# Optimization experiments

Measured on AMD Instinct MI355X. Metric: run time of the kernel, lower is better.

The kernel has to match this reference:

```python
import jax, jax.numpy as jnp
import numpy as np
from jax import lax

D_MODEL = 1024
D_STATE = 128
HEADDIM = 64
EXPAND = 2
NGROUPS = 1
CHUNK = 256
D_INNER = EXPAND * D_MODEL          # 2048
D_SSM = D_INNER                      # d_ssm defaults to d_inner
NHEADS = D_SSM // HEADDIM            # 32
CONV_DIM = D_SSM + 2 * NGROUPS * D_STATE   # 2304
D_IN_PROJ = 2 * D_INNER + 2 * NGROUPS * D_STATE + NHEADS  # 4384 -> d_mlp = 0
BATCH = 2
SEQLEN = 2048
EPS = 1e-5


def setup_inputs() -> dict:
    key = jax.random.key(0)
    ks = jax.random.split(key, 9)
    u = jax.random.normal(ks[0], (BATCH, SEQLEN, D_MODEL), jnp.float32)
    # indices into left-padded (len = SEQLEN+1) sequence; 0 selects the zero pad
    conv_indices = jax.random.randint(ks[1], (BATCH, 4 * SEQLEN), 0, SEQLEN + 1)
    W_in = jax.random.normal(ks[2], (D_IN_PROJ, D_MODEL), jnp.float32) / np.sqrt(D_MODEL).astype(np.float32)
    conv_w = jax.random.normal(ks[3], (CONV_DIM, 4), jnp.float32) * 0.2
    conv_b = jax.random.normal(ks[4], (CONV_DIM,), jnp.float32) * 0.02
    # dt_bias init exactly as the module: inverse-softplus of dt in [dt_min, dt_max]
    dt = jnp.exp(jax.random.uniform(ks[5], (NHEADS,), jnp.float32) * (np.log(0.1) - np.log(0.001)) + np.log(0.001))
    dt = jnp.clip(dt, 1e-4)
    dt_bias = dt + jnp.log(-jnp.expm1(-dt))
    A_log = jnp.log(jax.random.uniform(ks[6], (NHEADS,), jnp.float32, minval=1.0, maxval=16.0))
    D = jnp.ones((NHEADS,), jnp.float32)
    norm_w = jnp.ones((D_SSM,), jnp.float32)
    W_out = jax.random.normal(ks[7], (D_MODEL, D_INNER), jnp.float32) / np.sqrt(D_INNER).astype(np.float32)
    return dict(u=u, conv_indices=conv_indices, W_in=W_in, conv_w=conv_w, conv_b=conv_b,
                dt_bias=dt_bias, A_log=A_log, D=D, norm_w=norm_w, W_out=W_out)


def _segsum(x):
    # x: (b, c, h, cs) -> (b, c, h, cs, cs); out[..., t, s] = sum_{k=s+1..t} x[..., k]
    cs = x.shape[-1]
    cx = jnp.cumsum(x, axis=-1)
    diff = cx[..., :, None] - cx[..., None, :]
    mask = jnp.tril(jnp.ones((cs, cs), dtype=bool))
    return jnp.where(mask, diff, -jnp.inf)


def _ssd(x, dt, A, Bh, Ch, D):
    # Mamba2 SSD chunked scan. x:(b,l,h,p), dt:(b,l,h), A:(h,), Bh/Ch:(b,l,h,n), D:(h,)
    b, l, h, p = x.shape
    n = Bh.shape[-1]
    c = l // CHUNK
    xr = x.reshape(b, c, CHUNK, h, p)
    dtr = dt.reshape(b, c, CHUNK, h)
    Br = Bh.reshape(b, c, CHUNK, h, n)
    Cr = Ch.reshape(b, c, CHUNK, h, n)
    dA = dtr * A                                 # (b,c,cs,h)
    Acum = jnp.cumsum(dA, axis=2)                # (b,c,cs,h)
    Lm = jnp.exp(_segsum(jnp.transpose(dA, (0, 1, 3, 2))))  # (b,c,h,cs,cs)
    dtx = xr * dtr[..., None]                    # dt-weighted inputs
    # intra-chunk (diagonal blocks)
    Yd = jnp.einsum('bcthn,bcshn,bchts,bcshp->bcthp', Cr, Br, Lm, dtx)
    # per-chunk final states
    decay_states = jnp.exp(Acum[:, :, -1:, :] - Acum)        # (b,c,cs,h)
    states = jnp.einsum('bcshn,bcsh,bcshp->bchpn', Br, decay_states, dtx)
    chunk_decay = jnp.exp(Acum[:, :, -1, :])     # (b,c,h)
    def step(h_prev, inp):
        dec, st = inp
        return h_prev * dec[..., None, None] + st, h_prev
    init = jnp.zeros((b, h, p, n), x.dtype)
    _, prev = lax.scan(step, init, (jnp.moveaxis(chunk_decay, 1, 0), jnp.moveaxis(states, 1, 0)))
    prev = jnp.moveaxis(prev, 0, 1)              # (b,c,h,p,n): state entering each chunk
    # inter-chunk (off-diagonal) contribution
    Yoff = jnp.einsum('bcthn,bchpn,bcth->bcthp', Cr, prev, jnp.exp(Acum))
    Y = Yd + Yoff + D[None, None, None, :, None] * xr
    return Y.reshape(b, l, h, p)


def reference(u, conv_indices, W_in, conv_w, conv_b, dt_bias, A_log, D, norm_w, W_out):
    b, l, _ = u.shape
    zxbcdt = u @ W_in.T                          # (b,l,4384); d_mlp == 0
    z, xBC, dt_raw = jnp.split(zxbcdt, [D_SSM, D_SSM + CONV_DIM], axis=-1)
    # tree conv: left-pad seq by 1, gather 4 tree positions per output step, depthwise conv k=4 stride=4
    xc = jnp.transpose(xBC, (0, 2, 1))           # (b, conv_dim, l)
    xp = jnp.pad(xc, ((0, 0), (0, 0), (1, 0)))
    idx = jnp.broadcast_to(conv_indices[:, None, :], (b, CONV_DIM, 4 * l))
    g = jnp.take_along_axis(xp, idx, axis=2).reshape(b, CONV_DIM, l, 4)
    conv = jnp.einsum('bclk,ck->bcl', g, conv_w) + conv_b[None, :, None]
    xBC = jax.nn.silu(jnp.transpose(conv, (0, 2, 1)))  # (b,l,conv_dim)
    x, Bm, Cm = jnp.split(xBC, [D_SSM, D_SSM + NGROUPS * D_STATE], axis=-1)
    x = x.reshape(b, l, NHEADS, HEADDIM)
    hpg = NHEADS // NGROUPS
    Bh = jnp.repeat(Bm.reshape(b, l, NGROUPS, D_STATE), hpg, axis=2)
    Ch = jnp.repeat(Cm.reshape(b, l, NGROUPS, D_STATE), hpg, axis=2)
    dt = jax.nn.softplus(dt_raw + dt_bias)       # dt_softplus=True, default dt_limit
    A = -jnp.exp(A_log.astype(jnp.float32))
    y = _ssd(x, dt, A, Bh, Ch, D).reshape(b, l, D_SSM)
    # RMSNormGated, norm_before_gate=False, group_size = d_ssm (ngroups=1)
    yz = y * jax.nn.silu(z)
    var = jnp.mean(jnp.square(yz), axis=-1, keepdims=True)
    y = yz * lax.rsqrt(var + EPS) * norm_w
    return y @ W_out.T
```

## Files before the change

kernel.cpp:

```cpp
#include <hip/hip_runtime.h>

#define BB 2
#define LL 2048
#define DMODEL 1024
#define DSSM 2048
#define NH 32
#define HD 64
#define DST 128
#define CONVD 2304
#define DPROJ 4384
#define CS 64
#define NC 32
#define BLTOT (BB*LL)

typedef short v8s __attribute__((ext_vector_type(8)));
typedef float v4f __attribute__((ext_vector_type(4)));

__device__ __forceinline__ float b2f(unsigned short h) {
  union { unsigned int u; float f; } v; v.u = ((unsigned int)h) << 16; return v.f;
}
__device__ __forceinline__ unsigned short f2b(float f) {
  union { float f; unsigned int u; } v; v.f = f;
  unsigned int u = v.u;
  return (unsigned short)((u + 0x7fffu + ((u >> 16) & 1u)) >> 16);
}
__device__ __forceinline__ v4f mfma16(v8s a, v8s b, v4f c) {
  return __builtin_amdgcn_mfma_f32_16x16x32_bf16(a, b, c, 0, 0, 0);
}
__device__ __forceinline__ void gl_lds16(const unsigned short* g, unsigned short* l) {
  __builtin_amdgcn_global_load_lds(
      (const __attribute__((address_space(1))) void*)(g),
      (__attribute__((address_space(3))) void*)(l), 16, 0, 0);
}

__global__ __launch_bounds__(256) void cvt3_kernel(
    const float* __restrict__ a, unsigned short* __restrict__ oa, int na4,
    const float* __restrict__ b, unsigned short* __restrict__ ob, int nb4,
    const float* __restrict__ c, unsigned short* __restrict__ oc, int nc4)
{
  int i = blockIdx.x * 256 + threadIdx.x;
  const float* src; unsigned short* dst; int j;
  if (i < na4) { src = a; dst = oa; j = i; }
  else if (i < na4 + nb4) { src = b; dst = ob; j = i - na4; }
  else if (i < na4 + nb4 + nc4) { src = c; dst = oc; j = i - na4 - nb4; }
  else return;
  float4 v = ((const float4*)src)[j];
  ushort4 o;
  o.x = f2b(v.x); o.y = f2b(v.y); o.z = f2b(v.z); o.w = f2b(v.w);
  ((ushort4*)dst)[j] = o;
}

template<int TN, int OUT_BF16, int DBUF>
__global__ __launch_bounds__(256) void gemm_bt(
    const unsigned short* __restrict__ A, const unsigned short* __restrict__ Bt,
    void* __restrict__ Cout, int M, int N, int K, int ldc)
{
  constexpr int NT = TN / 32;
  constexpr int NB = DBUF ? 2 : 1;
  const int bm = blockIdx.x, bn = blockIdx.y;
  const int tid = threadIdx.x;
  const int wave = tid >> 6, lane = tid & 63;
  const int wm = wave & 1, wn = wave >> 1;
  const int q = lane >> 4, lr = lane & 15;

  __shared__ __align__(16) unsigned short As[NB][128 * 64];
  __shared__ __align__(16) unsigned short Bs[NB][TN * 64];

  v4f acc[4][NT];
#pragma unroll
  for (int i = 0; i < 4; i++)
#pragma unroll
    for (int j = 0; j < NT; j++) acc[i][j] = v4f{0.f, 0.f, 0.f, 0.f};

  const int lrow = lane >> 3;
  const int gchunk = (lane & 7) ^ lrow;

#define STAGE_TILE(bufi, k0) do {                                              \
    _Pragma("unroll")                                                          \
    for (int it = 0; it < 4; ++it) {                                           \
      int r = wave * 32 + it * 8 + lrow;                                       \
      gl_lds16(A + (size_t)(bm * 128 + r) * K + (k0) + gchunk * 8,             \
               &As[bufi][(wave * 32 + it * 8) * 64]);                          \
    }                                                                          \
    _Pragma("unroll")                                                          \
    for (int it = 0; it < TN / 32; ++it) {                                     \
      int rloc = wave * (TN / 4) + it * 8;                                     \
      int rb = bn * TN + rloc + lrow; if (rb >= N) rb = N - 1;                 \
      gl_lds16(Bt + (size_t)rb * K + (k0) + gchunk * 8, &Bs[bufi][rloc * 64]); \
    }                                                                          \
  } while (0)

#define COMPUTE_TILE(bufi) do {                                                \
    const unsigned short* __restrict__ Ab = As[bufi];                          \
    const unsigned short* __restrict__ Bb = Bs[bufi];                          \
    _Pragma("unroll")                                                          \
    for (int ks = 0; ks < 64; ks += 32) {                                      \
      const int c0 = (ks >> 3) + q;                                            \
      v8s af[4], bf[NT];                                                       \
      _Pragma("unroll")                                                        \
      for (int mt = 0; mt < 4; ++mt) {                                         \
        int r = wm * 64 + mt * 16 + lr;                                        \
        af[mt] = *(const v8s*)&Ab[r * 64 + ((c0 ^ (r & 7)) << 3)];             \
      }                                                                        \
      _Pragma("unroll")                                                        \
      for (int nt = 0; nt < NT; ++nt) {                                        \
        int r = wn * (TN / 2) + nt * 16 + lr;                                  \
        bf[nt] = *(const v8s*)&Bb[r * 64 + ((c0 ^ (r & 7)) << 3)];             \
      }                                                                        \
      _Pragma("unroll")                                                        \
      for (int mt = 0; mt < 4; ++mt)                                           \
        _Pragma("unroll")                                                      \
        for (int nt = 0; nt < NT; ++nt)                                        \
          acc[mt][nt] = mfma16(af[mt], bf[nt], acc[mt][nt]);                   \
    }                                                                          \
  } while (0)

#define WAIT_BARRIER() do {                                                    \
    __builtin_amdgcn_sched_barrier(0);                                         \
    asm volatile("s_waitcnt vmcnt(0) lgkmcnt(0)\ns_barrier" ::: "memory");     \
  } while (0)

  if constexpr (DBUF == 0) {
    for (int k0 = 0; k0 < K; k0 += 64) {
      __syncthreads();
      STAGE_TILE(0, k0);
      __syncthreads();
      COMPUTE_TILE(0);
    }
  } else {
    const int nkt = K >> 6;
    STAGE_TILE(0, 0);
    WAIT_BARRIER();
    for (int kt = 0; kt < nkt; ++kt) {
      const int cb = kt & 1;
      if (kt + 1 < nkt) STAGE_TILE(cb ^ 1, (kt + 1) << 6);
      COMPUTE_TILE(cb);
      if (kt + 1 < nkt) WAIT_BARRIER();
    }
  }
#undef STAGE_TILE
#undef COMPUTE_TILE
#undef WAIT_BARRIER

#pragma unroll
  for (int mt = 0; mt < 4; ++mt) {
#pragma unroll
    for (int nt = 0; nt < NT; ++nt) {
      int row = bm * 128 + wm * 64 + mt * 16 + q * 4;
      int col = bn * TN + wn * (TN / 2) + nt * 16 + lr;
      if (col < N) {
#pragma unroll
        for (int r = 0; r < 4; ++r) {
          float v = acc[mt][nt][r];
          if (OUT_BF16) ((unsigned short*)Cout)[(size_t)(row + r) * ldc + col] = f2b(v);
          else          ((float*)Cout)[(size_t)(row + r) * ldc + col] = v;
        }
      }
    }
  }
}

__global__ __launch_bounds__(256) void convBC_kernel(
    const unsigned short* __restrict__ C1, const int* __restrict__ cidx,
    const float* __restrict__ convw, const float* __restrict__ convb,
    const float* __restrict__ dtbias,
    unsigned short* __restrict__ Bg16, unsigned short* __restrict__ Cg16,
    unsigned short* __restrict__ BgT16, float* __restrict__ dtb)
{
  int bl0 = blockIdx.x * 16;
  int b = bl0 >> 11;
  int tid = threadIdx.x;
  __shared__ int idxs[64];
  if (tid < 64) {
    int tk = tid >> 2, k = tid & 3;
    idxs[tid] = cidx[b * (4 * LL) + (((bl0 + tk) & 2047) * 4) + k];
  }
  __syncthreads();
  const float4* cw4 = (const float4*)convw;
  int quad = tid & 63;
  int relc = DSSM + quad * 4;
  float4 w0 = cw4[relc], w1 = cw4[relc + 1], w2 = cw4[relc + 2], w3 = cw4[relc + 3];
  float4 cb = *(const float4*)(convb + relc);
  int tk0 = (tid >> 6) * 4;
  int cc = relc - DSSM;
  unsigned short btc[4][4];
#pragma unroll
  for (int tt = 0; tt < 4; ++tt) {
    int tk = tk0 + tt;
    int bl = bl0 + tk;
    ushort4 rv[4];
#pragma unroll
    for (int k = 0; k < 4; ++k) {
      int iv = idxs[tk * 4 + k];
      rv[k] = (iv > 0) ? *(const ushort4*)(C1 + (size_t)(b * LL + iv - 1) * DPROJ + DSSM + relc)
                       : make_ushort4(0, 0, 0, 0);
    }
    float a0 = cb.x + b2f(rv[0].x) * w0.x + b2f(rv[1].x) * w0.y + b2f(rv[2].x) * w0.z + b2f(rv[3].x) * w0.w;
    float a1 = cb.y + b2f(rv[0].y) * w1.x + b2f(rv[1].y) * w1.y + b2f(rv[2].y) * w1.z + b2f(rv[3].y) * w1.w;
    float a2 = cb.z + b2f(rv[0].z) * w2.x + b2f(rv[1].z) * w2.y + b2f(rv[2].z) * w2.z + b2f(rv[3].z) * w2.w;
    float a3 = cb.w + b2f(rv[0].w) * w3.x + b2f(rv[1].w) * w3.y + b2f(rv[2].w) * w3.z + b2f(rv[3].w) * w3.w;
    ushort4 o;
    o.x = f2b(a0 / (1.f + __expf(-a0)));
    o.y = f2b(a1 / (1.f + __expf(-a1)));
    o.z = f2b(a2 / (1.f + __expf(-a2)));
    o.w = f2b(a3 / (1.f + __expf(-a3)));
    if (cc < DST) {
      *(ushort4*)(Bg16 + (size_t)bl * DST + cc) = o;
      btc[0][tt] = o.x; btc[1][tt] = o.y; btc[2][tt] = o.z; btc[3][tt] = o.w;
    } else {
      *(ushort4*)(Cg16 + (size_t)bl * DST + (cc - DST)) = o;
    }
  }
  if (cc < DST) {
#pragma unroll
    for (int c = 0; c < 4; ++c)
      *(ushort4*)(BgT16 + (size_t)(cc + c) * BLTOT + bl0 + tk0) =
          make_ushort4(btc[c][0], btc[c][1], btc[c][2], btc[c][3]);
  }
  for (int u = tid; u < 16 * NH; u += 256) {
    int tk = u >> 5, hh = u & 31;
    int bl = bl0 + tk;
    float raw = b2f(C1[(size_t)bl * DPROJ + DSSM + CONVD + hh]) + dtbias[hh];
    float dtv = (raw > 20.f) ? raw : log1pf(__expf(raw));
    dtb[(size_t)bl * NH + hh] = dtv;
  }
}

__global__ __launch_bounds__(256) void d0_S(
    const unsigned short* __restrict__ Bg16, const unsigned short* __restrict__ Cg16,
    float* __restrict__ Sg)
{
  int gid = blockIdx.x;
  int tid = threadIdx.x, wave = tid >> 6, lane = tid & 63, q = lane >> 4, lr = lane & 15;
  __shared__ __align__(16) unsigned short Bn[CS * 136];
  const size_t blbase = (size_t)(gid >> 5) * LL + (gid & 31) * CS;
#pragma unroll
  for (int g = 0; g < 8; ++g) {
    int f = g * 256 + tid;
    int s = f >> 5, c4 = (f & 31) * 4;
    *(ushort4*)&Bn[s * 136 + c4] = *(const ushort4*)(Bg16 + (blbase + s) * DST + c4);
  }
  __syncthreads();
  v4f accS[4];
#pragma unroll
  for (int i = 0; i < 4; i++) accS[i] = v4f{0.f, 0.f, 0.f, 0.f};
#pragma unroll
  for (int ks = 0; ks < 128; ks += 32) {
    v8s a = *(const v8s*)(Cg16 + (blbase + wave * 16 + lr) * DST + ks + q * 8);
#pragma unroll
    for (int si = 0; si < 4; ++si) {
      v8s bb = *(const v8s*)&Bn[(si * 16 + lr) * 136 + ks + q * 8];
      accS[si] = mfma16(a, bb, accS[si]);
    }
  }
  float* So = Sg + (size_t)gid * (CS * CS);
#pragma unroll
  for (int si = 0; si < 4; ++si)
#pragma unroll
    for (int r = 0; r < 4; ++r)
      So[(wave * 16 + q * 4 + r) * CS + si * 16 + lr] = accS[si][r];
}

__global__ __launch_bounds__(256) void d1_intra(
    const unsigned short* __restrict__ C1, const int* __restrict__ cidx,
    const float* __restrict__ convw, const float* __restrict__ convb,
    const unsigned short* __restrict__ BgT16, const float* __restrict__ Sg,
    const float* __restrict__ dtb,
    const float* __restrict__ A_log, const float* __restrict__ Dp,
    unsigned short* __restrict__ y16, unsigned short* __restrict__ statesb,
    float* __restrict__ cdb, float* __restrict__ acumb)
{
  int gid = blockIdx.x;
  int h = gid & 31, ci = (gid >> 5) & 31, b = gid >> 10;
  int tid = threadIdx.x, wave = tid >> 6, lane = tid & 63, q = lane >> 4, lr = lane & 15;

  __shared__ __align__(16) unsigned short G[CS * 72];
  __shared__ __align__(16) unsigned short BTw[DST * 72];
  __shared__ __align__(16) unsigned short xT[HD * 72];
  __shared__ float dt_s[CS], ac_s[CS], dec_s[CS];
  __shared__ int idxs[CS * 4];
  __shared__ float wls[HD * 4];
  __shared__ float bls[HD];

  const size_t blbase = (size_t)b * LL + ci * CS;
  const size_t chbase = (size_t)(b * NC + ci) * NH + h;
  float Ah = -__expf(A_log[h]);

  if (wave == 0) {
    float d = dtb[(blbase + lane) * NH + h];
    float a = d * Ah;
#pragma unroll
    for (int off = 1; off < 64; off <<= 1) {
      float u = __shfl_up(a, off, 64);
      if (lane >= off) a += u;
    }
    float tot = __shfl(a, 63, 64);
    dt_s[lane] = d;
    ac_s[lane] = a;
    dec_s[lane] = __expf(tot - a);
    acumb[chbase * CS + lane] = a;
    if (lane == 0) cdb[chbase] = __expf(tot);
  }
  {
    int s = tid >> 2, k = tid & 3;
    idxs[tid] = cidx[b * (4 * LL) + (ci * CS + s) * 4 + k];
  }
  if (tid < HD) *(float4*)&wls[tid * 4] = *(const float4*)(convw + (h * HD + tid) * 4);
  if (tid < HD / 4) *(float4*)&bls[tid * 4] = *(const float4*)(convb + h * HD + tid * 4);
  __syncthreads();

#pragma unroll
  for (int g = 0; g < 8; ++g) {
    int f = g * 256 + tid;
    int n = f >> 4, s4 = (f & 15) * 4;
    ushort4 bv = *(const ushort4*)(BgT16 + (size_t)n * BLTOT + blbase + s4);
    ushort4 o;
    o.x = f2b(b2f(bv.x) * dec_s[s4 + 0] * dt_s[s4 + 0]);
    o.y = f2b(b2f(bv.y) * dec_s[s4 + 1] * dt_s[s4 + 1]);
    o.z = f2b(b2f(bv.z) * dec_s[s4 + 2] * dt_s[s4 + 2]);
    o.w = f2b(b2f(bv.w) * dec_s[s4 + 3] * dt_s[s4 + 3]);
    *(ushort4*)&BTw[n * 72 + s4] = o;
  }

#pragma unroll
  for (int g = 0; g < 4; ++g) {
    int f = g * 256 + tid;
    int s = f >> 4, p4 = (f & 15) * 4;
    ushort4 rv[4];
#pragma unroll
    for (int k = 0; k < 4; ++k) {
      int iv = idxs[s * 4 + k];
      rv[k] = (iv > 0) ? *(const ushort4*)(C1 + (size_t)(b * LL + iv - 1) * DPROJ + DSSM + h * HD + p4)
                       : make_ushort4(0, 0, 0, 0);
    }
    float4 w0 = *(const float4*)&wls[(p4 + 0) * 4];
    float4 w1 = *(const float4*)&wls[(p4 + 1) * 4];
    float4 w2 = *(const float4*)&wls[(p4 + 2) * 4];
    float4 w3 = *(const float4*)&wls[(p4 + 3) * 4];
    float a0 = bls[p4 + 0] + b2f(rv[0].x) * w0.x + b2f(rv[1].x) * w0.y + b2f(rv[2].x) * w0.z + b2f(rv[3].x) * w0.w;
    float a1 = bls[p4 + 1] + b2f(rv[0].y) * w1.x + b2f(rv[1].y) * w1.y + b2f(rv[2].y) * w1.z + b2f(rv[3].y) * w1.w;
    float a2 = bls[p4 + 2] + b2f(rv[0].z) * w2.x + b2f(rv[1].z) * w2.y + b2f(rv[2].z) * w2.z + b2f(rv[3].z) * w2.w;
    float a3 = bls[p4 + 3] + b2f(rv[0].w) * w3.x + b2f(rv[1].w) * w3.y + b2f(rv[2].w) * w3.z + b2f(rv[3].w) * w3.w;
    xT[(p4 + 0) * 72 + s] = f2b(a0 / (1.f + __expf(-a0)));
    xT[(p4 + 1) * 72 + s] = f2b(a1 / (1.f + __expf(-a1)));
    xT[(p4 + 2) * 72 + s] = f2b(a2 / (1.f + __expf(-a2)));
    xT[(p4 + 3) * 72 + s] = f2b(a3 / (1.f + __expf(-a3)));
  }

  {
    const float* Sc = Sg + (size_t)(b * NC + ci) * (CS * CS);
    int tbase = wave * 16 + q * 4;
#pragma unroll
    for (int si = 0; si < 4; ++si) {
      int s = si * 16 + lr;
      float ds = dt_s[s], as = ac_s[s];
#pragma unroll
      for (int r = 0; r < 4; ++r) {
        int tt = tbase + r;
        float g = 0.f;
        if (s <= tt) g = Sc[tt * CS + s] * __expf(ac_s[tt] - as) * ds;
        G[tt * 72 + s] = f2b(g);
      }
    }
  }
  __syncthreads();

  v4f accY[4], accPT[4][2];
#pragma unroll
  for (int i = 0; i < 4; i++) {
    accY[i] = v4f{0.f,0.f,0.f,0.f};
    accPT[i][0] = v4f{0.f,0.f,0.f,0.f};
    accPT[i][1] = v4f{0.f,0.f,0.f,0.f};
  }
  int nw = wave * 32;
#pragma unroll
  for (int ks = 0; ks < 64; ks += 32) {
    v8s xf[4];
#pragma unroll
    for (int i = 0; i < 4; ++i) xf[i] = *(const v8s*)&xT[(i * 16 + lr) * 72 + ks + q * 8];
    v8s aG  = *(const v8s*)&G[(wave * 16 + lr) * 72 + ks + q * 8];
    v8s bw0 = *(const v8s*)&BTw[(nw + lr) * 72 + ks + q * 8];
    v8s bw1 = *(const v8s*)&BTw[(nw + 16 + lr) * 72 + ks + q * 8];
#pragma unroll
    for (int nt = 0; nt < 4; ++nt) {
      accY[nt] = mfma16(aG, xf[nt], accY[nt]);
      accPT[nt][0] = mfma16(xf[nt], bw0, accPT[nt][0]);
      accPT[nt][1] = mfma16(xf[nt], bw1, accPT[nt][1]);
    }
  }

  float Dh = Dp[h];
#pragma unroll
  for (int nt = 0; nt < 4; ++nt) {
    int p = nt * 16 + lr;
#pragma unroll
    for (int r = 0; r < 4; ++r) {
      int t = wave * 16 + q * 4 + r;
      float xv = b2f(xT[p * 72 + t]);
      y16[(blbase + t) * DSSM + h * HD + p] = f2b(accY[nt][r] + Dh * xv);
    }
  }
  size_t sbase = chbase * (DST * HD);
#pragma unroll
  for (int mt = 0; mt < 4; ++mt) {
#pragma unroll
    for (int nt = 0; nt < 2; ++nt) {
      int n = nw + nt * 16 + lr;
#pragma unroll
      for (int r = 0; r < 4; ++r) {
        int p = mt * 16 + q * 4 + r;
        statesb[sbase + (size_t)p * DST + n] = f2b(accPT[mt][nt][r]);
      }
    }
  }
}

__global__ __launch_bounds__(256) void d2_scan(
    unsigned short* __restrict__ statesb, const float* __restrict__ cdb)
{
  int g = blockIdx.x;
  int seg = g & 7, bh = g >> 3;
  int b = bh >> 5, h = bh & 31;
  int e4 = seg * 1024 + threadIdx.x * 4;
  const size_t cstride = (size_t)NH * DST * HD;
  size_t base = ((size_t)(b * NC) * NH + h) * (DST * HD) + e4;
  ushort4 st[NC];
#pragma unroll
  for (int ci = 0; ci < NC; ++ci) st[ci] = *(const ushort4*)(statesb + base + ci * cstride);
  float r0 = 0.f, r1 = 0.f, r2 = 0.f, r3 = 0.f;
#pragma unroll
  for (int ci = 0; ci < NC; ++ci) {
    float cd = cdb[(b * NC + ci) * NH + h];
    *(ushort4*)(statesb + base + ci * cstride) =
        make_ushort4(f2b(r0), f2b(r1), f2b(r2), f2b(r3));
    r0 = r0 * cd + b2f(st[ci].x);
    r1 = r1 * cd + b2f(st[ci].y);
    r2 = r2 * cd + b2f(st[ci].z);
    r3 = r3 * cd + b2f(st[ci].w);
  }
}

__global__ __launch_bounds__(256) void d3_inter(
    const unsigned short* __restrict__ Cg16,
    const unsigned short* __restrict__ statesb, const float* __restrict__ acumb,
    unsigned short* __restrict__ y16)
{
  int gid = blockIdx.x;
  int h = gid & 31, ci = (gid >> 5) & 31, b = gid >> 10;
  int tid = threadIdx.x, wave = tid >> 6, lane = tid & 63, q = lane >> 4, lr = lane & 15;
  __shared__ __align__(16) unsigned short pT[HD * 136];
  __shared__ __align__(16) float ys[CS * 68];
  __shared__ float ea[CS];
  const size_t blbase = (size_t)b * LL + ci * CS;
  const size_t chbase = (size_t)(b * NC + ci) * NH + h;
  if (tid < CS) ea[tid] = __expf(acumb[chbase * CS + tid]);
  size_t sbase = chbase * (DST * HD);
#pragma unroll
  for (int g = 0; g < 8; ++g) {
    int f = g * 256 + tid;
    int p = f >> 5, c4 = (f & 31) * 4;
    *(ushort4*)&pT[p * 136 + c4] = *(const ushort4*)(statesb + sbase + (size_t)p * DST + c4);
  }
  __syncthreads();
  v4f acc[4];
#pragma unroll
  for (int i = 0; i < 4; i++) acc[i] = v4f{0.f, 0.f, 0.f, 0.f};
#pragma unroll
  for (int ks = 0; ks < 128; ks += 32) {
    v8s a = *(const v8s*)(Cg16 + (blbase + wave * 16 + lr) * DST + ks + q * 8);
#pragma unroll
    for (int nt = 0; nt < 4; ++nt) {
      v8s bb = *(const v8s*)&pT[(nt * 16 + lr) * 136 + ks + q * 8];
      acc[nt] = mfma16(a, bb, acc[nt]);
    }
  }
#pragma unroll
  for (int nt = 0; nt < 4; ++nt) {
#pragma unroll
    for (int r = 0; r < 4; ++r)
      ys[(wave * 16 + q * 4 + r) * 68 + nt * 16 + lr] = acc[nt][r];
  }
  __syncthreads();
#pragma unroll
  for (int it = 0; it < 2; ++it) {
    int unit = it * 256 + tid;
    int t = unit >> 3, p8 = (unit & 7) * 8;
    float ea_t = ea[t];
    size_t off = (blbase + t) * DSSM + h * HD + p8;
    uint4 yv = *(const uint4*)(y16 + off);
    float4 o0 = *(const float4*)&ys[t * 68 + p8];
    float4 o1 = *(const float4*)&ys[t * 68 + p8 + 4];
    const unsigned int* yu = (const unsigned int*)&yv;
    float oo[8] = {o0.x, o0.y, o0.z, o0.w, o1.x, o1.y, o1.z, o1.w};
    unsigned int ro[4];
#pragma unroll
    for (int d = 0; d < 4; ++d) {
      unsigned short y0 = (unsigned short)(yu[d] & 0xffffu), y1 = (unsigned short)(yu[d] >> 16);
      float v0 = b2f(y0) + ea_t * oo[d * 2 + 0];
      float v1 = b2f(y1) + ea_t * oo[d * 2 + 1];
      ro[d] = (unsigned int)f2b(v0) | ((unsigned int)f2b(v1) << 16);
    }
    *(uint4*)(y16 + off) = make_uint4(ro[0], ro[1], ro[2], ro[3]);
  }
}

__global__ __launch_bounds__(256) void norm_kernel(
    const unsigned short* __restrict__ y16, const unsigned short* __restrict__ C1,
    const float* __restrict__ normw, unsigned short* __restrict__ yzn)
{
  int bl = blockIdx.x;
  int tid = threadIdx.x;
  int wave = tid >> 6, lane = tid & 63;
  int c8 = tid * 8;
  uint4 yv = *(const uint4*)(y16 + (size_t)bl * DSSM + c8);
  uint4 zv = *(const uint4*)(C1 + (size_t)bl * DPROJ + c8);
  const unsigned int* yu = (const unsigned int*)&yv;
  const unsigned int* zu = (const unsigned int*)&zv;
  float vals[8];
  float ss = 0.f;
#pragma unroll
  for (int d = 0; d < 4; ++d) {
    unsigned short y0 = (unsigned short)(yu[d] & 0xffffu), y1 = (unsigned short)(yu[d] >> 16);
    unsigned short z0 = (unsigned short)(zu[d] & 0xffffu), z1 = (unsigned short)(zu[d] >> 16);
    float zf0 = b2f(z0), zf1 = b2f(z1);
    float v0 = b2f(y0) * (zf0 / (1.f + __expf(-zf0)));
    float v1 = b2f(y1) * (zf1 / (1.f + __expf(-zf1)));
    vals[d * 2] = v0; vals[d * 2 + 1] = v1;
    ss += v0 * v0 + v1 * v1;
  }
#pragma unroll
  for (int off = 32; off > 0; off >>= 1) ss += __shfl_down(ss, off);
  __shared__ float red[4];
  if (lane == 0) red[wave] = ss;
  __syncthreads();
  float tot = red[0] + red[1] + red[2] + red[3];
  float scale = rsqrtf(tot * (1.f / 2048.f) + 1e-5f);
  float4 w0 = *(const float4*)(normw + c8);
  float4 w1 = *(const float4*)(normw + c8 + 4);
  float ws[8] = {w0.x, w0.y, w0.z, w0.w, w1.x, w1.y, w1.z, w1.w};
  unsigned int ro[4];
#pragma unroll
  for (int d = 0; d < 4; ++d) {
    unsigned short r0 = f2b(vals[d * 2] * scale * ws[d * 2]);
    unsigned short r1 = f2b(vals[d * 2 + 1] * scale * ws[d * 2 + 1]);
    ro[d] = (unsigned int)r0 | ((unsigned int)r1 << 16);
  }
  *(uint4*)(yzn + (size_t)bl * DSSM + c8) = make_uint4(ro[0], ro[1], ro[2], ro[3]);
}

extern "C" void kernel_launch(void* const* d_in, const int* in_sizes, int n_in,
                              void* d_out, int out_size, void* d_ws, size_t ws_size,
                              hipStream_t stream) {
  const float* u      = (const float*)d_in[0];
  const int*   cidx   = (const int*)d_in[1];
  const float* W_in   = (const float*)d_in[2];
  const float* convw  = (const float*)d_in[3];
  const float* convb  = (const float*)d_in[4];
  const float* dtbias = (const float*)d_in[5];
  const float* A_log  = (const float*)d_in[6];
  const float* Dp     = (const float*)d_in[7];
  const float* normw  = (const float*)d_in[8];
  const float* W_out  = (const float*)d_in[9];

  char* w = (char*)d_ws;
  size_t off = 0;
  auto alloc = [&](size_t bytes) { char* p = w + off; off += (bytes + 255) & ~(size_t)255; return p; };
  unsigned short* u16     = (unsigned short*)alloc((size_t)BLTOT * DMODEL * 2);
  unsigned short* Win16   = (unsigned short*)alloc((size_t)DPROJ * DMODEL * 2);
  unsigned short* Wout16  = (unsigned short*)alloc((size_t)DMODEL * DSSM * 2);
  unsigned short* C1      = (unsigned short*)alloc((size_t)BLTOT * DPROJ * 2);
  unsigned short* Bg16    = (unsigned short*)alloc((size_t)BLTOT * DST * 2);
  unsigned short* Cg16    = (unsigned short*)alloc((size_t)BLTOT * DST * 2);
  unsigned short* BgT16   = (unsigned short*)alloc((size_t)DST * BLTOT * 2);
  float*          Sg      = (float*)alloc((size_t)BB * NC * CS * CS * 4);
  float*          dtb     = (float*)alloc((size_t)BLTOT * NH * 4);
  float*          acumb   = (float*)alloc((size_t)BB * NC * NH * CS * 4);
  unsigned short* y16     = (unsigned short*)alloc((size_t)BLTOT * DSSM * 2);
  unsigned short* statesb = (unsigned short*)alloc((size_t)BB * NC * NH * DST * HD * 2);
  float*          cdb     = (float*)alloc((size_t)BB * NC * NH * 4);
  unsigned short* yzn     = (unsigned short*)alloc((size_t)BLTOT * DSSM * 2);

  const int na4 = BLTOT * DMODEL / 4, nb4 = DPROJ * DMODEL / 4, nc4 = DMODEL * DSSM / 4;
  cvt3_kernel<<<(na4 + nb4 + nc4 + 255) / 256, 256, 0, stream>>>(
      u, u16, na4, W_in, Win16, nb4, W_out, Wout16, nc4);

  gemm_bt<128, 1, 0><<<dim3(BLTOT / 128, (DPROJ + 127) / 128), 256, 0, stream>>>(
      u16, Win16, C1, BLTOT, DPROJ, DMODEL, DPROJ);
  convBC_kernel<<<BLTOT / 16, 256, 0, stream>>>(C1, cidx, convw, convb, dtbias,
                                                Bg16, Cg16, BgT16, dtb);
  d0_S<<<BB * NC, 256, 0, stream>>>(Bg16, Cg16, Sg);
  d1_intra<<<BB * NC * NH, 256, 0, stream>>>(C1, cidx, convw, convb, BgT16, Sg,
                                             dtb, A_log, Dp, y16, statesb, cdb, acumb);
  d2_scan<<<BB * NH * 8, 256, 0, stream>>>(statesb, cdb);
  d3_inter<<<BB * NC * NH, 256, 0, stream>>>(Cg16, statesb, acumb, y16);
  norm_kernel<<<BLTOT, 256, 0, stream>>>(y16, C1, normw, yzn);
  gemm_bt<64, 0, 1><<<dim3(BLTOT / 128, DMODEL / 64), 256, 0, stream>>>(
      yzn, Wout16, (float*)d_out, BLTOT, DMODEL, DSSM, DMODEL);
}
```

Measured before the change: 254.5 us.

## Fuse inter-chunk state scan with inter-chunk output contribution kernel

Merges the separate state-passing scan and the inter-chunk C·state output kernel into one kernel. Each 64-thread block keeps a running state slice in registers and, chunk by chunk, feeds it directly into MFMA to update y, so the scanned states are never written back and reread. The cost is a serial 32-chunk loop per block with only 1024 single-wave blocks. The y read-modify-writes also become scalar bf16 accesses, and each block recomputes the Cg loads.

```diff
diff --git a/kernel.cpp b/kernel.cpp
--- a/kernel.cpp
+++ b/kernel.cpp
@@ -415,92 +415,55 @@
   }
 }
 
-__global__ __launch_bounds__(256) void d2_scan(
-    unsigned short* __restrict__ statesb, const float* __restrict__ cdb)
-{
-  int g = blockIdx.x;
-  int seg = g & 7, bh = g >> 3;
-  int b = bh >> 5, h = bh & 31;
-  int e4 = seg * 1024 + threadIdx.x * 4;
+__global__ __launch_bounds__(64) void d23_scan_inter(
+    const unsigned short* __restrict__ Cg16,
+    const unsigned short* __restrict__ statesb,
+    const float* __restrict__ acumb, const float* __restrict__ cdb,
+    unsigned short* __restrict__ y16)
+{
+  int gid = blockIdx.x;
+  int tq = gid & 3, pq = (gid >> 2) & 3, h = (gid >> 4) & 31, b = gid >> 9;
+  int lane = threadIdx.x, q = lane >> 4, lr = lane & 15;
   const size_t cstride = (size_t)NH * DST * HD;
-  size_t base = ((size_t)(b * NC) * NH + h) * (DST * HD) + e4;
-  ushort4 st[NC];
-#pragma unroll
-  for (int ci = 0; ci < NC; ++ci) st[ci] = *(const ushort4*)(statesb + base + ci * cstride);
-  float r0 = 0.f, r1 = 0.f, r2 = 0.f, r3 = 0.f;
-#pragma unroll
+  const size_t srow = ((size_t)(b * NC) * NH + h) * (DST * HD)
+                    + (size_t)(pq * 16 + lr) * DST;
+
+  float run[4][8];
+#pragma unroll
+  for (int ks = 0; ks < 4; ++ks)
+#pragma unroll
+    for (int j = 0; j < 8; ++j) run[ks][j] = 0.f;
+
   for (int ci = 0; ci < NC; ++ci) {
-    float cd = cdb[(b * NC + ci) * NH + h];
-    *(ushort4*)(statesb + base + ci * cstride) =
-        make_ushort4(f2b(r0), f2b(r1), f2b(r2), f2b(r3));
-    r0 = r0 * cd + b2f(st[ci].x);
-    r1 = r1 * cd + b2f(st[ci].y);
-    r2 = r2 * cd + b2f(st[ci].z);
-    r3 = r3 * cd + b2f(st[ci].w);
-  }
-}
-
-__global__ __launch_bounds__(256) void d3_inter(
-    const unsigned short* __restrict__ Cg16,
-    const unsigned short* __restrict__ statesb, const float* __restrict__ acumb,
-    unsigned short* __restrict__ y16)
-{
-  int gid = blockIdx.x;
-  int h = gid & 31, ci = (gid >> 5) & 31, b = gid >> 10;
-  int tid = threadIdx.x, wave = tid >> 6, lane = tid & 63, q = lane >> 4, lr = lane & 15;
-  __shared__ __align__(16) unsigned short pT[HD * 136];
-  __shared__ __align__(16) float ys[CS * 68];
-  __shared__ float ea[CS];
-  const size_t blbase = (size_t)b * LL + ci * CS;
-  const size_t chbase = (size_t)(b * NC + ci) * NH + h;
-  if (tid < CS) ea[tid] = __expf(acumb[chbase * CS + tid]);
-  size_t sbase = chbase * (DST * HD);
-#pragma unroll
-  for (int g = 0; g < 8; ++g) {
-    int f = g * 256 + tid;
-    int p = f >> 5, c4 = (f & 31) * 4;
-    *(ushort4*)&pT[p * 136 + c4] = *(const ushort4*)(statesb + sbase + (size_t)p * DST + c4);
-  }
-  __syncthreads();
-  v4f acc[4];
-#pragma unroll
-  for (int i = 0; i < 4; i++) acc[i] = v4f{0.f, 0.f, 0.f, 0.f};
-#pragma unroll
-  for (int ks = 0; ks < 128; ks += 32) {
-    v8s a = *(const v8s*)(Cg16 + (blbase + wave * 16 + lr) * DST + ks + q * 8);
-#pragma unroll
-    for (int nt = 0; nt < 4; ++nt) {
-      v8s bb = *(const v8s*)&pT[(nt * 16 + lr) * 136 + ks + q * 8];
-      acc[nt] = mfma16(a, bb, acc[nt]);
-    }
-  }
-#pragma unroll
-  for (int nt = 0; nt < 4; ++nt) {
-#pragma unroll
-    for (int r = 0; r < 4; ++r)
-      ys[(wave * 16 + q * 4 + r) * 68 + nt * 16 + lr] = acc[nt][r];
-  }
-  __syncthreads();
-#pragma unroll
-  for (int it = 0; it < 2; ++it) {
-    int unit = it * 256 + tid;
-    int t = unit >> 3, p8 = (unit & 7) * 8;
-    float ea_t = ea[t];
-    size_t off = (blbase + t) * DSSM + h * HD + p8;
-    uint4 yv = *(const uint4*)(y16 + off);
-    float4 o0 = *(const float4*)&ys[t * 68 + p8];
-    float4 o1 = *(const float4*)&ys[t * 68 + p8 + 4];
-    const unsigned int* yu = (const unsigned int*)&yv;
-    float oo[8] = {o0.x, o0.y, o0.z, o0.w, o1.x, o1.y, o1.z, o1.w};
-    unsigned int ro[4];
-#pragma unroll
-    for (int d = 0; d < 4; ++d) {
-      unsigned short y0 = (unsigned short)(yu[d] & 0xffffu), y1 = (unsigned short)(yu[d] >> 16);
-      float v0 = b2f(y0) + ea_t * oo[d * 2 + 0];
-      float v1 = b2f(y1) + ea_t * oo[d * 2 + 1];
-      ro[d] = (unsigned int)f2b(v0) | ((unsigned int)f2b(v1) << 16);
-    }
-    *(uint4*)(y16 + off) = make_uint4(ro[0], ro[1], ro[2], ro[3]);
+    const size_t chbase = (size_t)(b * NC + ci) * NH + h;
+    const size_t blbase = (size_t)b * LL + ci * CS;
+    v8s bf[4];
+#pragma unroll
+    for (int ks = 0; ks < 4; ++ks)
+#pragma unroll
+      for (int j = 0; j < 8; ++j) bf[ks][j] = (short)f2b(run[ks][j]);
+    v4f acc = v4f{0.f, 0.f, 0.f, 0.f};
+#pragma unroll
+    for (int ks = 0; ks < 4; ++ks) {
+      v8s a = *(const v8s*)(Cg16 + (blbase + tq * 16 + lr) * DST + ks * 32 + q * 8);
+      acc = mfma16(a, bf[ks], acc);
+    }
+    float4 eav = *(const float4*)(acumb + chbase * CS + tq * 16 + q * 4);
+    float ea[4] = {__expf(eav.x), __expf(eav.y), __expf(eav.z), __expf(eav.w)};
+#pragma unroll
+    for (int r = 0; r < 4; ++r) {
+      int t = tq * 16 + q * 4 + r;
+      size_t off = (blbase + t) * DSSM + h * HD + pq * 16 + lr;
+      y16[off] = f2b(b2f(y16[off]) + ea[r] * acc[r]);
+    }
+    float cd = cdb[chbase];
+#pragma unroll
+    for (int ks = 0; ks < 4; ++ks) {
+      v8s st = *(const v8s*)(statesb + srow + ci * cstride + ks * 32 + q * 8);
+#pragma unroll
+      for (int j = 0; j < 8; ++j)
+        run[ks][j] = run[ks][j] * cd + b2f((unsigned short)st[j]);
+    }
   }
 }
 
@@ -591,8 +554,7 @@
   d0_S<<<BB * NC, 256, 0, stream>>>(Bg16, Cg16, Sg);
   d1_intra<<<BB * NC * NH, 256, 0, stream>>>(C1, cidx, convw, convb, BgT16, Sg,
                                              dtb, A_log, Dp, y16, statesb, cdb, acumb);
-  d2_scan<<<BB * NH * 8, 256, 0, stream>>>(statesb, cdb);
-  d3_inter<<<BB * NC * NH, 256, 0, stream>>>(Cg16, statesb, acumb, y16);
+  d23_scan_inter<<<BB * NH * 16, 64, 0, stream>>>(Cg16, statesb, acumb, cdb, y16);
   norm_kernel<<<BLTOT, 256, 0, stream>>>(y16, C1, normw, yzn);
   gemm_bt<64, 0, 1><<<dim3(BLTOT / 128, DMODEL / 64), 256, 0, stream>>>(
       yzn, Wout16, (float*)d_out, BLTOT, DMODEL, DSSM, DMODEL);
```

After: 281.4 us. 1.11x slower.
